# Kernel optimization log

Measured on AMD Instinct MI355X. Metric: run time of the kernel, lower is better.

The kernel has to match this reference:

```python
import jax, jax.numpy as jnp
import numpy as np

N_UNITS = 100
N_INPUTS = 7
N_OUTPUTS = 1
T = 60
STIM_ON, STIM_OFF = 10, 15
RESP_START, RESP_END = 20, 35
REWARD_DURATION = 5
ALPHA = 0.2            # dt / tau = 100 / 500
SIGMA_REC = 0.15
B = 8192


def setup_inputs() -> dict:
    key = jax.random.key(0)
    k1, k2, k3, k4, k5, k6, k7 = jax.random.split(key, 7)
    W_in_raw = (jax.random.normal(k1, (N_UNITS, N_INPUTS)) * 0.05).astype(jnp.float32)
    W_rec_np = np.asarray(jax.random.normal(k2, (N_UNITS, N_UNITS))) / np.sqrt(N_UNITS)
    sr = float(np.abs(np.linalg.eigvals(W_rec_np)).max())
    W_rec = jnp.asarray(W_rec_np * (0.8 / sr), dtype=jnp.float32)
    b_rec = jnp.zeros((N_UNITS,), jnp.float32)
    w_out = (jax.random.normal(k3, (N_OUTPUTS, N_UNITS)) * 0.1).astype(jnp.float32)
    b_out = jnp.zeros((N_OUTPUTS,), jnp.float32)
    return {
        "y0": jnp.zeros((B, N_UNITS), jnp.float32),
        "noise": jax.random.normal(k4, (B, T, N_UNITS), dtype=jnp.float32),
        "stimulus_idx": jax.random.randint(k5, (B,), 0, 4).astype(jnp.int32),
        "rewarded_target_idx": jax.random.randint(k6, (B,), 0, 4).astype(jnp.int32),
        "instruction": jax.random.randint(k7, (B,), 0, 2).astype(jnp.int32),
        "W_in_raw": W_in_raw, "W_rec": W_rec, "b_rec": b_rec,
        "w_out": w_out, "b_out": b_out,
    }


def reference(y0, noise, stimulus_idx, rewarded_target_idx, instruction,
              W_in_raw, W_rec, b_rec, w_out, b_out):
    W_in = jnp.abs(W_in_raw)               # [N, n_in]
    w_lick = W_in[:, 5]
    w_reward = W_in[:, 4]
    noise_scale = SIGMA_REC * float(np.sqrt(2.0 * ALPHA))
    t_idx = jnp.arange(T, dtype=jnp.int32)
    stim_mask = ((t_idx >= STIM_ON) & (t_idx < STIM_OFF)).astype(jnp.float32)
    resp_mask = ((t_idx >= RESP_START) & (t_idx < RESP_END)).astype(jnp.float32)
    auto_start = RESP_END - REWARD_DURATION

    def trial(y0_i, eps_i, stim, rew, instr):
        is_rew = stim == rew
        instr_b = instr > 0
        # base open-loop input: stimulus channel + response cue (channel 6)
        u_base = jnp.zeros((T, N_INPUTS), jnp.float32).at[:, 6].set(resp_mask)
        u_base = u_base + stim_mask[:, None] * jax.nn.one_hot(stim, N_INPUTS, dtype=jnp.float32)
        wu = u_base @ W_in.T + b_rec        # [T, N]

        def step(carry, xs):
            y, licked, lick_t, instr_fired = carry
            t, wu_t, eps_t = xs
            # instruction auto-reward fires at auto_start if no reward yet (applied BEFORE pre)
            delivered = instr_fired | (licked & is_rew)
            fire = instr_b & (~delivered) & (t == auto_start)
            instr_fired = instr_fired | fire
            instr_active = instr_fired & (t >= auto_start) & (t < RESP_END)
            # lick-triggered inputs affect dynamics only AFTER the lick step (wu[t] already consumed)
            lick_dyn = licked & (t > lick_t) & (t < lick_t + REWARD_DURATION)
            add = (instr_active.astype(jnp.float32) + (lick_dyn & is_rew).astype(jnp.float32)) * w_reward \
                  + lick_dyn.astype(jnp.float32) * w_lick
            pre = y @ W_rec.T + wu_t + add + noise_scale * eps_t
            y = (1.0 - ALPHA) * y + ALPHA * jax.nn.relu(pre)
            z = jax.nn.sigmoid(y @ w_out.T + b_out)[0]
            # closed-loop lick decision (after readout)
            in_resp = (t >= RESP_START) & (t < RESP_END)
            trig = in_resp & (~licked) & (z > 0.5)
            lick_t = jnp.where(trig, t, lick_t)
            licked = licked | trig
            # u_trial markings include the lick step itself
            u5 = licked & (t >= lick_t) & (t < lick_t + REWARD_DURATION)
            u4 = instr_active | (u5 & is_rew)
            return (y, licked, lick_t, instr_fired), (z, u5, u4)

        init = (y0_i, jnp.array(False), jnp.array(T + 1, jnp.int32), jnp.array(False))
        (yf, licked, lick_t, instr_fired), (z_seq, u5, u4) = jax.lax.scan(
            step, init, (t_idx, wu, eps_i))
        u = u_base.at[:, 5].set(u5.astype(jnp.float32)).at[:, 4].set(u4.astype(jnp.float32))
        reward_delivered = instr_fired | (licked & is_rew)
        target = jnp.where(is_rew, resp_mask, jnp.zeros_like(resp_mask))
        return u, target, resp_mask > 0, licked, reward_delivered, z_seq, yf

    return jax.vmap(trial)(y0, noise, stimulus_idx, rewarded_target_idx, instruction)
```

## Files before the change

### kernel.cpp

```cpp
#include <hip/hip_runtime.h>
#include <math.h>

#define BB 8192
#define TT 60
#define NU 100
#define NI 7

typedef float v2f __attribute__((ext_vector_type(2)));
typedef float v4f __attribute__((ext_vector_type(4)));


#define FOR25(M) M(0) M(1) M(2) M(3) M(4) M(5) M(6) M(7) M(8) M(9) \
  M(10) M(11) M(12) M(13) M(14) M(15) M(16) M(17) M(18) M(19) \
  M(20) M(21) M(22) M(23) M(24)

#define RL(v,l) __int_as_float(__builtin_amdgcn_readlane(__float_as_int(v), l))

#define DPPADD(ctrl, rmask) { \
  const int _t = __builtin_amdgcn_update_dpp(0, __float_as_int(part), (ctrl), (rmask), 0xf, false); \
  part += __int_as_float(_t); }

#define TRIAL_SETUP(s) \
  const int  trial##s  = tbase + s; \
  const int  stim##s   = stim_idx[trial##s]; \
  const bool isrew##s  = (stim##s == rew_idx[trial##s]); \
  const bool instrb##s = (instr_in[trial##s] > 0); \
  const v2f  wis##s = { fabsf(W_in_raw[ua * NI + stim##s]), fabsf(W_in_raw[(ua+1) * NI + stim##s]) }; \
  v2f  yy##s = ((const v2f*)(y0 + trial##s * NU))[la]; \
  bool licked##s = false, fired##s = false; \
  int  lickt##s = TT + 1; \
  const float* nbase##s = noise + trial##s * (TT * NU); \
  v2f  en##s = ((const v2f*)nbase##s)[la];

#define PUBLISH(s) ((v2f*)&lds_y[wid * 4 + s][0])[la] = yy##s;

#define DECLACC(s) v2f aX0_##s = {0,0}, aX1_##s = {0,0}, aY0_##s = {0,0}, aY1_##s = {0,0};

#define MACQ(s, j2) { \
  const v4f q = Y##s[j2]; \
  aX0_##s += (v2f){q.x, q.y} * wx0; \
  aY0_##s += (v2f){q.x, q.y} * wy0; \
  aX1_##s += (v2f){q.z, q.w} * wx1; \
  aY1_##s += (v2f){q.z, q.w} * wy1; }

#define MACJ2(j2) { \
  const v2f wx0 = wX[(2*(j2)    ) * 50 + la]; \
  const v2f wx1 = wX[(2*(j2) + 1) * 50 + la]; \
  const v2f wy0 = wY[(2*(j2)    ) * 50 + la]; \
  const v2f wy1 = wY[(2*(j2) + 1) * 50 + la]; \
  MACQ(0, j2) MACQ(1, j2) MACQ(2, j2) MACQ(3, j2) }

#define TAILA(s, t, sm, rm) { \
  const v2f e = en##s; \
  en##s = ((const v2f*)(nbase##s + tn * NU))[la]; \
  const bool dl = fired##s || (licked##s && isrew##s); \
  const bool fr = instrb##s && !dl && ((t) == 30); \
  fired##s = fired##s || fr; \
  ia##s = fired##s && ((t) >= 30) && ((t) < 35); \
  const bool ld = licked##s && ((t) > lickt##s) && ((t) < lickt##s + 5); \
  const float ar = (ia##s ? 1.0f : 0.0f) + ((ld && isrew##s) ? 1.0f : 0.0f); \
  const float al = ld ? 1.0f : 0.0f; \
  const v2f base = br + (rm) * wi6 + (sm) * wis##s + ar * wr + al * wl + NS * e; \
  const v2f sX = aX0_##s + aX1_##s; \
  const v2f sY = aY0_##s + aY1_##s; \
  const v2f pre  = base + (v2f){ sX.x + sX.y, sY.x + sY.y }; \
  const v2f prer = { fmaxf(pre.x, 0.0f), fmaxf(pre.y, 0.0f) }; \
  yy##s = 0.8f * yy##s + 0.2f * prer; }

#define ZED(s, t) { \
  float part = yy##s.x * wo.x + yy##s.y * wo.y; \
  DPPADD(0x111, 0xf) DPPADD(0x112, 0xf) DPPADD(0x114, 0xf) DPPADD(0x118, 0xf) \
  DPPADD(0x142, 0xa) DPPADD(0x143, 0xc) \
  const float xx = RL(part, 63) + bo; \
  z##s = 1.0f / (1.0f + expf(-xx)); \
  const bool inr  = ((t) >= 20) && ((t) < 35); \
  const bool trig = inr && !licked##s && (z##s > 0.5f); \
  if (trig) lickt##s = (t); \
  licked##s = licked##s || trig; \
  u5##s = licked##s && ((t) >= lickt##s) && ((t) < lickt##s + 5); \
  u4##s = ia##s || (u5##s && isrew##s); }

#define FSTORE(s, t, sm, rm) { \
  const int bt = trial##s * TT + (t); \
  if (lane < NI) { \
    float uv = 0.0f; \
    if (lane == stim##s) uv = (sm); \
    if (lane == 4) uv = u4##s ? 1.0f : 0.0f; \
    if (lane == 5) uv = u5##s ? 1.0f : 0.0f; \
    if (lane == 6) uv = (rm); \
    uout[bt * NI + lane] = uv; \
  } else if (lane == 8) { tout[bt] = isrew##s ? (rm) : 0.0f; } \
  else if (lane == 9)   { rout[bt] = (rm); } \
  else if (lane == 10)  { zout[bt] = z##s; } }

__global__ __launch_bounds__(256, 2)
void drr_kernel(const float* __restrict__ y0,
                const float* __restrict__ noise,
                const int*   __restrict__ stim_idx,
                const int*   __restrict__ rew_idx,
                const int*   __restrict__ instr_in,
                const float* __restrict__ W_in_raw,
                const float* __restrict__ W_rec,
                const float* __restrict__ b_rec,
                const float* __restrict__ w_out,
                const float* __restrict__ b_out,
                float* __restrict__ out)
{
    const int tid   = threadIdx.x;
    const int lane  = tid & 63;
    const int wid   = tid >> 6;
    const int tbase = blockIdx.x * 16 + wid * 4;

    const bool act = (lane < 50);
    const int  la  = act ? lane : 49;
    const int  ua  = 2 * la;

    __shared__ v2f wtX[2500];
    __shared__ v2f wtY[2500];
    __shared__ v4f lds_y[16][26];

    for (int idx = tid; idx < 2500; idx += 256) {
        const int j = idx / 50, l = idx % 50;
        wtX[idx] = *(const v2f*)(W_rec + (2 * l)     * NU + 2 * j);
        wtY[idx] = *(const v2f*)(W_rec + (2 * l + 1) * NU + 2 * j);
    }
    __syncthreads();

    const v2f wi6 = { fabsf(W_in_raw[ua * NI + 6]), fabsf(W_in_raw[(ua+1) * NI + 6]) };
    const v2f wr  = { fabsf(W_in_raw[ua * NI + 4]), fabsf(W_in_raw[(ua+1) * NI + 4]) };
    const v2f wl  = { fabsf(W_in_raw[ua * NI + 5]), fabsf(W_in_raw[(ua+1) * NI + 5]) };
    const v2f br  = { b_rec[ua], b_rec[ua + 1] };
    const v2f wo  = act ? (v2f){ w_out[ua], w_out[ua + 1] } : (v2f){ 0.0f, 0.0f };
    const float bo = b_out[0];
    const float NS = 0.09486832980505138f;

    TRIAL_SETUP(0) TRIAL_SETUP(1) TRIAL_SETUP(2) TRIAL_SETUP(3)

    const v4f* Y0 = &lds_y[wid * 4 + 0][0];
    const v4f* Y1 = &lds_y[wid * 4 + 1][0];
    const v4f* Y2 = &lds_y[wid * 4 + 2][0];
    const v4f* Y3 = &lds_y[wid * 4 + 3][0];

    float* uout  = out;
    float* tout  = out  + BB * TT * NI;
    float* rout  = tout + BB * TT;
    float* lout  = rout + BB * TT;
    float* dout  = lout + BB;
    float* zout  = dout + BB;
    float* yfout = zout + BB * TT;

    for (int t = 0; t < TT; ++t) {
        unsigned wofs = 0;
        asm volatile("" : "+v"(wofs));
        const v2f* wX = (const v2f*)wtX + wofs;
        const v2f* wY = (const v2f*)wtY + wofs;

        PUBLISH(0) PUBLISH(1) PUBLISH(2) PUBLISH(3)

        DECLACC(0) DECLACC(1) DECLACC(2) DECLACC(3)

        FOR25(MACJ2)

        const int tn = (t < TT - 1) ? t + 1 : t;
        const float sm = (t >= 10 && t < 15) ? 1.0f : 0.0f;
        const float rm = (t >= 20 && t < 35) ? 1.0f : 0.0f;

        bool ia0, ia1, ia2, ia3;
        float z0, z1, z2, z3;
        bool u40, u41, u42, u43, u50, u51, u52, u53;

        TAILA(0, t, sm, rm) TAILA(1, t, sm, rm)
        TAILA(2, t, sm, rm) TAILA(3, t, sm, rm)

        ZED(0, t) ZED(1, t) ZED(2, t) ZED(3, t)

        FSTORE(0, t, sm, rm) FSTORE(1, t, sm, rm)
        FSTORE(2, t, sm, rm) FSTORE(3, t, sm, rm)
    }

    if (lane == 0) {
        lout[trial0] = licked0 ? 1.0f : 0.0f;
        dout[trial0] = (fired0 || (licked0 && isrew0)) ? 1.0f : 0.0f;
        lout[trial1] = licked1 ? 1.0f : 0.0f;
        dout[trial1] = (fired1 || (licked1 && isrew1)) ? 1.0f : 0.0f;
        lout[trial2] = licked2 ? 1.0f : 0.0f;
        dout[trial2] = (fired2 || (licked2 && isrew2)) ? 1.0f : 0.0f;
        lout[trial3] = licked3 ? 1.0f : 0.0f;
        dout[trial3] = (fired3 || (licked3 && isrew3)) ? 1.0f : 0.0f;
    }
    if (act) {
        ((v2f*)(yfout + trial0 * NU))[la] = yy0;
        ((v2f*)(yfout + trial1 * NU))[la] = yy1;
        ((v2f*)(yfout + trial2 * NU))[la] = yy2;
        ((v2f*)(yfout + trial3 * NU))[la] = yy3;
    }
}

extern "C" void kernel_launch(void* const* d_in, const int* in_sizes, int n_in,
                              void* d_out, int out_size, void* d_ws, size_t ws_size,
                              hipStream_t stream) {
    const float* y0       = (const float*)d_in[0];
    const float* noise    = (const float*)d_in[1];
    const int*   stim     = (const int*)  d_in[2];
    const int*   rew      = (const int*)  d_in[3];
    const int*   instr    = (const int*)  d_in[4];
    const float* W_in_raw = (const float*)d_in[5];
    const float* W_rec    = (const float*)d_in[6];
    const float* b_rec    = (const float*)d_in[7];
    const float* w_out    = (const float*)d_in[8];
    const float* b_out    = (const float*)d_in[9];
    float* out = (float*)d_out;

    drr_kernel<<<BB / 16, 256, 0, stream>>>(y0, noise, stim, rew, instr,
                                            W_in_raw, W_rec, b_rec, w_out, b_out, out);
}
```

Measured before the change: 508.4 us.

## Broadcast hidden state via readlane instead of LDS round-trip in recurrent matvec

Each step's hidden state is no longer written to LDS and read back as v4f. Each lane's y values are now broadcast with v_readlane into scalar registers and used as scalar operands of fmaf. The two weight tables are merged into a single interleaved v4f table, so each j iteration needs one 128-bit LDS load. The noise prefetch moves to the top of the loop. This removes LDS writes and y reads and the dependency on LDS latency, at the cost of 400 readlanes per step, which may serialize on the SALU and force scalar-register pressure.

```diff
diff --git a/kernel.cpp b/kernel.cpp
--- a/kernel.cpp
+++ b/kernel.cpp
@@ -10,9 +10,11 @@
 typedef float v4f __attribute__((ext_vector_type(4)));
 
 
-#define FOR25(M) M(0) M(1) M(2) M(3) M(4) M(5) M(6) M(7) M(8) M(9) \
+#define FOR50(M) M(0) M(1) M(2) M(3) M(4) M(5) M(6) M(7) M(8) M(9) \
   M(10) M(11) M(12) M(13) M(14) M(15) M(16) M(17) M(18) M(19) \
-  M(20) M(21) M(22) M(23) M(24)
+  M(20) M(21) M(22) M(23) M(24) M(25) M(26) M(27) M(28) M(29) \
+  M(30) M(31) M(32) M(33) M(34) M(35) M(36) M(37) M(38) M(39) \
+  M(40) M(41) M(42) M(43) M(44) M(45) M(46) M(47) M(48) M(49)
 
 #define RL(v,l) __int_as_float(__builtin_amdgcn_readlane(__float_as_int(v), l))
 
@@ -32,27 +34,27 @@
   const float* nbase##s = noise + trial##s * (TT * NU); \
   v2f  en##s = ((const v2f*)nbase##s)[la];
 
-#define PUBLISH(s) ((v2f*)&lds_y[wid * 4 + s][0])[la] = yy##s;
-
-#define DECLACC(s) v2f aX0_##s = {0,0}, aX1_##s = {0,0}, aY0_##s = {0,0}, aY1_##s = {0,0};
-
-#define MACQ(s, j2) { \
-  const v4f q = Y##s[j2]; \
-  aX0_##s += (v2f){q.x, q.y} * wx0; \
-  aY0_##s += (v2f){q.x, q.y} * wy0; \
-  aX1_##s += (v2f){q.z, q.w} * wx1; \
-  aY1_##s += (v2f){q.z, q.w} * wy1; }
-
-#define MACJ2(j2) { \
-  const v2f wx0 = wX[(2*(j2)    ) * 50 + la]; \
-  const v2f wx1 = wX[(2*(j2) + 1) * 50 + la]; \
-  const v2f wy0 = wY[(2*(j2)    ) * 50 + la]; \
-  const v2f wy1 = wY[(2*(j2) + 1) * 50 + la]; \
-  MACQ(0, j2) MACQ(1, j2) MACQ(2, j2) MACQ(3, j2) }
+#define PREF(s) const v2f e##s = en##s; \
+  en##s = ((const v2f*)(nbase##s + tn * NU))[la];
+
+#define DECLACC(s) float aAe##s = 0.0f, aAo##s = 0.0f, aBe##s = 0.0f, aBo##s = 0.0f;
+
+#define MACJ(j) { \
+  const v4f w = wC[(j) * 50 + la]; \
+  const float ya0 = RL(yy0.x, j), yb0 = RL(yy0.y, j); \
+  const float ya1 = RL(yy1.x, j), yb1 = RL(yy1.y, j); \
+  const float ya2 = RL(yy2.x, j), yb2 = RL(yy2.y, j); \
+  const float ya3 = RL(yy3.x, j), yb3 = RL(yy3.y, j); \
+  aAe0 = fmaf(w.x, ya0, aAe0); aAo0 = fmaf(w.y, yb0, aAo0); \
+  aBe0 = fmaf(w.z, ya0, aBe0); aBo0 = fmaf(w.w, yb0, aBo0); \
+  aAe1 = fmaf(w.x, ya1, aAe1); aAo1 = fmaf(w.y, yb1, aAo1); \
+  aBe1 = fmaf(w.z, ya1, aBe1); aBo1 = fmaf(w.w, yb1, aBo1); \
+  aAe2 = fmaf(w.x, ya2, aAe2); aAo2 = fmaf(w.y, yb2, aAo2); \
+  aBe2 = fmaf(w.z, ya2, aBe2); aBo2 = fmaf(w.w, yb2, aBo2); \
+  aAe3 = fmaf(w.x, ya3, aAe3); aAo3 = fmaf(w.y, yb3, aAo3); \
+  aBe3 = fmaf(w.z, ya3, aBe3); aBo3 = fmaf(w.w, yb3, aBo3); }
 
 #define TAILA(s, t, sm, rm) { \
-  const v2f e = en##s; \
-  en##s = ((const v2f*)(nbase##s + tn * NU))[la]; \
   const bool dl = fired##s || (licked##s && isrew##s); \
   const bool fr = instrb##s && !dl && ((t) == 30); \
   fired##s = fired##s || fr; \
@@ -60,10 +62,8 @@
   const bool ld = licked##s && ((t) > lickt##s) && ((t) < lickt##s + 5); \
   const float ar = (ia##s ? 1.0f : 0.0f) + ((ld && isrew##s) ? 1.0f : 0.0f); \
   const float al = ld ? 1.0f : 0.0f; \
-  const v2f base = br + (rm) * wi6 + (sm) * wis##s + ar * wr + al * wl + NS * e; \
-  const v2f sX = aX0_##s + aX1_##s; \
-  const v2f sY = aY0_##s + aY1_##s; \
-  const v2f pre  = base + (v2f){ sX.x + sX.y, sY.x + sY.y }; \
+  const v2f base = br + (rm) * wi6 + (sm) * wis##s + ar * wr + al * wl + NS * e##s; \
+  const v2f pre  = base + (v2f){ aAe##s + aAo##s, aBe##s + aBo##s }; \
   const v2f prer = { fmaxf(pre.x, 0.0f), fmaxf(pre.y, 0.0f) }; \
   yy##s = 0.8f * yy##s + 0.2f * prer; }
 
@@ -115,14 +115,15 @@
     const int  la  = act ? lane : 49;
     const int  ua  = 2 * la;
 
-    __shared__ v2f wtX[2500];
-    __shared__ v2f wtY[2500];
-    __shared__ v4f lds_y[16][26];
-
-    for (int idx = tid; idx < 2500; idx += 256) {
-        const int j = idx / 50, l = idx % 50;
-        wtX[idx] = *(const v2f*)(W_rec + (2 * l)     * NU + 2 * j);
-        wtY[idx] = *(const v2f*)(W_rec + (2 * l + 1) * NU + 2 * j);
+    __shared__ v4f wtC[2500];
+
+    {
+        v2f* wt2 = (v2f*)wtC;
+        for (int idx = tid; idx < 2500; idx += 256) {
+            const int j = idx / 50, l = idx % 50;
+            wt2[2 * idx]     = *(const v2f*)(W_rec + (2 * l)     * NU + 2 * j);
+            wt2[2 * idx + 1] = *(const v2f*)(W_rec + (2 * l + 1) * NU + 2 * j);
+        }
     }
     __syncthreads();
 
@@ -136,11 +137,6 @@
 
     TRIAL_SETUP(0) TRIAL_SETUP(1) TRIAL_SETUP(2) TRIAL_SETUP(3)
 
-    const v4f* Y0 = &lds_y[wid * 4 + 0][0];
-    const v4f* Y1 = &lds_y[wid * 4 + 1][0];
-    const v4f* Y2 = &lds_y[wid * 4 + 2][0];
-    const v4f* Y3 = &lds_y[wid * 4 + 3][0];
-
     float* uout  = out;
     float* tout  = out  + BB * TT * NI;
     float* rout  = tout + BB * TT;
@@ -150,18 +146,17 @@
     float* yfout = zout + BB * TT;
 
     for (int t = 0; t < TT; ++t) {
+        const int tn = (t < TT - 1) ? t + 1 : t;
+        PREF(0) PREF(1) PREF(2) PREF(3)
+
         unsigned wofs = 0;
         asm volatile("" : "+v"(wofs));
-        const v2f* wX = (const v2f*)wtX + wofs;
-        const v2f* wY = (const v2f*)wtY + wofs;
-
-        PUBLISH(0) PUBLISH(1) PUBLISH(2) PUBLISH(3)
+        const v4f* wC = (const v4f*)wtC + wofs;
 
         DECLACC(0) DECLACC(1) DECLACC(2) DECLACC(3)
 
-        FOR25(MACJ2)
-
-        const int tn = (t < TT - 1) ? t + 1 : t;
+        FOR50(MACJ)
+
         const float sm = (t >= 10 && t < 15) ? 1.0f : 0.0f;
         const float rm = (t >= 20 && t < 35) ? 1.0f : 0.0f;
 
```

New measurement: 565.8 us. 1.11x slower.
